# Kernel tuning notes

Hardware: AMD Instinct MI355X
Metric: run time of the kernel (lower is better)

## Reference

```python
import jax, jax.numpy as jnp
import numpy as np

N_EMBD = 1024
N_HEAD = 16
HEAD_DIM = N_EMBD // N_HEAD
B, T = 4, 1024
EPS = 1e-5


def _linear_params(key, fan_in, fan_out):
    kw, kb = jax.random.split(key)
    bound = 1.0 / np.sqrt(fan_in)
    W = jax.random.uniform(kw, (fan_in, fan_out), minval=-bound, maxval=bound, dtype=jnp.float32)
    b = jax.random.uniform(kb, (fan_out,), minval=-bound, maxval=bound, dtype=jnp.float32)
    return W, b


def setup_inputs() -> dict:
    key = jax.random.key(0)
    ks = jax.random.split(key, 8)
    x = jax.random.normal(ks[0], (B, T, N_EMBD), dtype=jnp.float32)
    Wq, bq = _linear_params(ks[1], N_EMBD, N_EMBD)
    Wk, bk = _linear_params(ks[2], N_EMBD, N_EMBD)
    Wv, bv = _linear_params(ks[3], N_EMBD, N_EMBD)
    Wp, bp = _linear_params(ks[4], N_EMBD, N_EMBD)
    W1, b1 = _linear_params(ks[5], N_EMBD, 4 * N_EMBD)
    W2, b2 = _linear_params(ks[6], 4 * N_EMBD, N_EMBD)
    g1 = jnp.ones((N_EMBD,), jnp.float32); be1 = jnp.zeros((N_EMBD,), jnp.float32)
    g2 = jnp.ones((N_EMBD,), jnp.float32); be2 = jnp.zeros((N_EMBD,), jnp.float32)
    return {"x": x, "Wq": Wq, "bq": bq, "Wk": Wk, "bk": bk, "Wv": Wv, "bv": bv,
            "Wp": Wp, "bp": bp, "W1": W1, "b1": b1, "W2": W2, "b2": b2,
            "g1": g1, "be1": be1, "g2": g2, "be2": be2}


def _layernorm(x, g, b):
    mu = jnp.mean(x, axis=-1, keepdims=True)
    var = jnp.mean(jnp.square(x - mu), axis=-1, keepdims=True)
    return (x - mu) * jax.lax.rsqrt(var + EPS) * g + b


def _attention(x, Wq, bq, Wk, bk, Wv, bv, Wp, bp):
    Bsz, Tt, C = x.shape
    def heads(W, b):
        return (x @ W + b).reshape(Bsz, Tt, N_HEAD, HEAD_DIM).transpose(0, 2, 1, 3)  # [B,H,T,d]
    q, k, v = heads(Wq, bq), heads(Wk, bk), heads(Wv, bv)
    scores = jnp.einsum('bhqd,bhkd->bhqk', q, k) / np.sqrt(HEAD_DIM).astype(np.float32)
    causal = jnp.tril(jnp.ones((Tt, Tt), dtype=bool))
    scores = jnp.where(causal, scores, -jnp.inf)
    attn = jax.nn.softmax(scores, axis=-1)
    out = jnp.einsum('bhqk,bhkd->bhqd', attn, v)  # [B,H,T,d]
    out = out.transpose(0, 2, 1, 3).reshape(Bsz, Tt, C)
    return out @ Wp + bp


def _ff(x, W1, b1, W2, b2):
    h = jax.nn.gelu(x @ W1 + b1, approximate=False)  # torch nn.GELU default = exact erf
    return h @ W2 + b2


def reference(x, Wq, bq, Wk, bk, Wv, bv, Wp, bp, W1, b1, W2, b2, g1, be1, g2, be2):
    x = x + _attention(_layernorm(x, g1, be1), Wq, bq, Wk, bk, Wv, bv, Wp, bp)
    x = x + _ff(_layernorm(x, g2, be2), W1, b1, W2, b2)
    return x
```

## Files before the change

kernel.cpp:

```cpp
#include <hip/hip_runtime.h>
#include <hip/hip_bf16.h>

typedef __attribute__((ext_vector_type(8))) __bf16 bf16x8;
typedef __attribute__((ext_vector_type(4))) float f32x4;
typedef __attribute__((ext_vector_type(4))) unsigned short u16x4;
typedef unsigned short u16;

#define AS3(p) ((__attribute__((address_space(3))) void*)(p))
#define AS1(p) ((const __attribute__((address_space(1))) void*)(p))

#define QSCALE 0.18033688011112042f

__device__ __forceinline__ u16 f2b(float f) {
    __hip_bfloat16 h = __float2bfloat16(f);
    return __builtin_bit_cast(u16, h);
}

__device__ __forceinline__ float gelu_exact(float v) {
    const float z = v * 0.70710678118654752f;
    const float a = fabsf(z);
    const float t = __builtin_amdgcn_rcpf(1.0f + 0.3275911f * a);
    float p = 1.061405429f;
    p = p * t - 1.453152027f;
    p = p * t + 1.421413741f;
    p = p * t - 0.284496736f;
    p = p * t + 0.254829592f;
    p = p * t;
    float erfv = 1.0f - p * __expf(-a * a);
    erfv = copysignf(erfv, z);
    return 0.5f * v * (1.0f + erfv);
}

__global__ __launch_bounds__(256) void transpose_w(
    const float* __restrict__ W, u16* __restrict__ WT, int K, int N)
{
    __shared__ u16 tile[32][33];
    const int tx = threadIdx.x & 31, ty = threadIdx.x >> 5;
    const int n0 = blockIdx.x * 32, k0 = blockIdx.y * 32;
    #pragma unroll
    for (int p = 0; p < 4; ++p)
        tile[ty + p * 8][tx] = f2b(W[(size_t)(k0 + ty + p * 8) * N + n0 + tx]);
    __syncthreads();
    #pragma unroll
    for (int p = 0; p < 4; ++p)
        WT[(size_t)(n0 + ty + p * 8) * K + k0 + tx] = tile[tx][ty + p * 8];
}

__global__ __launch_bounds__(256) void transpose_w3(
    const float* __restrict__ W0, const float* __restrict__ W1,
    const float* __restrict__ W2, u16* __restrict__ WT)
{
    __shared__ u16 tile[32][33];
    const int z = blockIdx.z;
    const float* W = (z == 0) ? W0 : (z == 1) ? W1 : W2;
    u16* dst = WT + (size_t)z * 1024 * 1024;
    const int tx = threadIdx.x & 31, ty = threadIdx.x >> 5;
    const int n0 = blockIdx.x * 32, k0 = blockIdx.y * 32;
    #pragma unroll
    for (int p = 0; p < 4; ++p)
        tile[ty + p * 8][tx] = f2b(W[(size_t)(k0 + ty + p * 8) * 1024 + n0 + tx]);
    __syncthreads();
    #pragma unroll
    for (int p = 0; p < 4; ++p)
        dst[(size_t)(n0 + ty + p * 8) * 1024 + k0 + tx] = tile[tx][ty + p * 8];
}

__global__ __launch_bounds__(256) void ln_bf16(
    const float* __restrict__ xin, const float* __restrict__ gam,
    const float* __restrict__ bet, u16* __restrict__ yout)
{
    __shared__ float red[8];
    const int row = blockIdx.x, tid = threadIdx.x;
    float4 v = ((const float4*)(xin + (size_t)row * 1024))[tid];
    float s = v.x + v.y + v.z + v.w;
    #pragma unroll
    for (int o = 32; o > 0; o >>= 1) s += __shfl_xor(s, o, 64);
    if ((tid & 63) == 0) red[tid >> 6] = s;
    __syncthreads();
    const float mu = (red[0] + red[1] + red[2] + red[3]) * (1.f / 1024.f);
    const float dx = v.x - mu, dy = v.y - mu, dz = v.z - mu, dw = v.w - mu;
    float sq = dx * dx + dy * dy + dz * dz + dw * dw;
    #pragma unroll
    for (int o = 32; o > 0; o >>= 1) sq += __shfl_xor(sq, o, 64);
    if ((tid & 63) == 0) red[4 + (tid >> 6)] = sq;
    __syncthreads();
    const float var = (red[4] + red[5] + red[6] + red[7]) * (1.f / 1024.f);
    const float inv = rsqrtf(var + 1e-5f);
    const float4 G = ((const float4*)gam)[tid];
    const float4 Bt = ((const float4*)bet)[tid];
    u16x4 o;
    o[0] = f2b(dx * inv * G.x + Bt.x);
    o[1] = f2b(dy * inv * G.y + Bt.y);
    o[2] = f2b(dz * inv * G.z + Bt.z);
    o[3] = f2b(dw * inv * G.w + Bt.w);
    ((u16x4*)(yout + (size_t)row * 1024))[tid] = o;
}

__global__ __launch_bounds__(256) void reduce_ln(
    const float* __restrict__ p0, const float* __restrict__ p1,
    const float* __restrict__ bias, const float* __restrict__ resid,
    const float* __restrict__ gam, const float* __restrict__ bet,
    float* __restrict__ xout, u16* __restrict__ yout)
{
    __shared__ float red[8];
    const int row = blockIdx.x, tid = threadIdx.x;
    const size_t off = (size_t)row * 256 + tid;
    float4 a = ((const float4*)p0)[off];
    const float4 b = ((const float4*)p1)[off];
    const float4 r = ((const float4*)resid)[off];
    const float4 bs = ((const float4*)bias)[tid];
    a.x += b.x + r.x + bs.x; a.y += b.y + r.y + bs.y;
    a.z += b.z + r.z + bs.z; a.w += b.w + r.w + bs.w;
    ((float4*)xout)[off] = a;
    float s = a.x + a.y + a.z + a.w;
    #pragma unroll
    for (int o = 32; o > 0; o >>= 1) s += __shfl_xor(s, o, 64);
    if ((tid & 63) == 0) red[tid >> 6] = s;
    __syncthreads();
    const float mu = (red[0] + red[1] + red[2] + red[3]) * (1.f / 1024.f);
    const float dx = a.x - mu, dy = a.y - mu, dz = a.z - mu, dw = a.w - mu;
    float sq = dx * dx + dy * dy + dz * dz + dw * dw;
    #pragma unroll
    for (int o = 32; o > 0; o >>= 1) sq += __shfl_xor(sq, o, 64);
    if ((tid & 63) == 0) red[4 + (tid >> 6)] = sq;
    __syncthreads();
    const float var = (red[4] + red[5] + red[6] + red[7]) * (1.f / 1024.f);
    const float inv = rsqrtf(var + 1e-5f);
    const float4 G = ((const float4*)gam)[tid];
    const float4 Bt = ((const float4*)bet)[tid];
    u16x4 o;
    o[0] = f2b(dx * inv * G.x + Bt.x);
    o[1] = f2b(dy * inv * G.y + Bt.y);
    o[2] = f2b(dz * inv * G.z + Bt.z);
    o[3] = f2b(dw * inv * G.w + Bt.w);
    ((u16x4*)(yout + (size_t)row * 1024))[tid] = o;
}

__global__ __launch_bounds__(256) void reduce_add(
    const float* __restrict__ p0, const float* __restrict__ p1,
    const float* __restrict__ bias, const float* __restrict__ resid,
    float* __restrict__ out)
{
    const size_t i = (size_t)blockIdx.x * 256 + threadIdx.x;
    float4 a = ((const float4*)p0)[i];
    const float4 b = ((const float4*)p1)[i];
    const float4 r = ((const float4*)resid)[i];
    const float4 bs = ((const float4*)bias)[i & 255];
    a.x += b.x + r.x + bs.x; a.y += b.y + r.y + bs.y;
    a.z += b.z + r.z + bs.z; a.w += b.w + r.w + bs.w;
    ((float4*)out)[i] = a;
}

template <int MODE, int BM, int SK>
__global__ __launch_bounds__(256, (BM == 128 ? 3 : 2)) void gemm_bf16(
    const u16* __restrict__ A, const u16* __restrict__ BT,
    const float* __restrict__ b0, const float* __restrict__ b1,
    const float* __restrict__ b2,
    void* __restrict__ outp, int M, int N, int K)
{
    constexpr int WM = BM / 2;
    constexpr int MI = WM / 16;
    constexpr int NI = 4;
    constexpr int AJ = BM / 64;
    constexpr int AELEM = BM * 32;
    constexpr int BELEM = 128 * 32;
    __shared__ u16 Asm[3 * AELEM];
    __shared__ u16 Bsm[3 * BELEM];

    const int tid = threadIdx.x;
    const int lane = tid & 63, wid = tid >> 6;
    const int wm = wid >> 1, wn = wid & 1;
    const int g = lane >> 4, l16 = lane & 15;
    const int sx = (l16 >> 1) & 3;
    const int sslot = (lane & 3) ^ ((lane >> 3) & 3);

    const int nBN = N >> 7;
    const int per = (M / BM) * nBN;
    const int cpx = gridDim.x >> 3;
    const int wg = (blockIdx.x & 7) * cpx + (blockIdx.x >> 3);
    const int skid = (SK > 1) ? (wg / per) : 0;
    const int rem = wg - skid * per;
    const int bm0 = (rem / nBN) * BM, bn0 = (rem % nBN) * 128;
    const int kb = skid * (K / SK);

    f32x4 acc[MI][NI] = {};

    const u16* aBase = A + (size_t)(bm0 + (lane >> 2)) * K + kb + sslot * 8;
    const u16* bBase = BT + (size_t)(bn0 + (lane >> 2)) * K + kb + sslot * 8;

    auto stage = [&](int kt, int buf) {
        u16* adst = Asm + buf * AELEM + lane * 8;
        u16* bdst = Bsm + buf * BELEM + lane * 8;
        #pragma unroll
        for (int j = 0; j < AJ; ++j) {
            const int ia = wid * AJ + j;
            __builtin_amdgcn_global_load_lds(AS1(aBase + (size_t)(ia * 16) * K + kt),
                                             AS3(adst + ia * 512), 16, 0, 0);
        }
        #pragma unroll
        for (int j = 0; j < 2; ++j) {
            const int ib = wid * 2 + j;
            __builtin_amdgcn_global_load_lds(AS1(bBase + (size_t)(ib * 16) * K + kt),
                                             AS3(bdst + ib * 512), 16, 0, 0);
        }
    };

    const int nt = K / (32 * SK);
    stage(0, 0);
    stage(32, 1);
    int cur = 0, pre = 2;

    for (int t = 0; t < nt; ++t) {
        if (t + 1 < nt) {
            if constexpr (BM == 256) asm volatile("s_waitcnt vmcnt(6)" ::: "memory");
            else                     asm volatile("s_waitcnt vmcnt(4)" ::: "memory");
        } else {
            asm volatile("s_waitcnt vmcnt(0)" ::: "memory");
        }
        __builtin_amdgcn_s_barrier();
        __builtin_amdgcn_sched_barrier(0);

        const u16* asrc = Asm + cur * AELEM;
        const u16* bsrc = Bsm + cur * BELEM;
        bf16x8 af[MI], bfr[NI];
        #pragma unroll
        for (int mi = 0; mi < MI; ++mi) {
            const int r = wm * WM + mi * 16 + l16;
            af[mi] = *(const bf16x8*)(asrc + r * 32 + ((g ^ sx) << 3));
        }
        #pragma unroll
        for (int ni = 0; ni < NI; ++ni) {
            const int c = wn * 64 + ni * 16 + l16;
            bfr[ni] = *(const bf16x8*)(bsrc + c * 32 + ((g ^ sx) << 3));
        }
        if (t + 2 < nt) stage((t + 2) * 32, pre);

        #pragma unroll
        for (int mi = 0; mi < MI; ++mi)
            #pragma unroll
            for (int ni = 0; ni < NI; ++ni)
                acc[mi][ni] = __builtin_amdgcn_mfma_f32_16x16x32_bf16(
                    af[mi], bfr[ni], acc[mi][ni], 0, 0, 0);

        pre = cur;
        cur = (cur == 2) ? 0 : cur + 1;
    }

    #pragma unroll
    for (int mi = 0; mi < MI; ++mi) {
        #pragma unroll
        for (int ni = 0; ni < NI; ++ni) {
            #pragma unroll
            for (int j = 0; j < 4; ++j) {
                const int m = bm0 + wm * WM + mi * 16 + g * 4 + j;
                const int n = bn0 + wn * 64 + ni * 16 + l16;
                float v = acc[mi][ni][j];
                if constexpr (MODE == 0) {
                    const float bias = (n < 1024) ? b0[n]
                                      : (n < 2048) ? b1[n - 1024] : b2[n - 2048];
                    float o = v + bias;
                    if (n < 1024) o *= QSCALE;
                    ((u16*)outp)[(size_t)m * N + n] = f2b(o);
                } else if constexpr (MODE == 2) {
                    ((u16*)outp)[(size_t)m * N + n] = f2b(gelu_exact(v + b0[n]));
                } else {
                    float* pout = (float*)outp + (size_t)skid * M * N;
                    pout[(size_t)m * N + n] = v;
                }
            }
        }
    }
}

__global__ __launch_bounds__(256) void attn_fwd(
    const u16* __restrict__ qkv, u16* __restrict__ outp)
{
    __shared__ u16 Ksm[2][64 * 64];
    __shared__ u16 Vsm[2][64 * 64];
    __shared__ u16 Psm[4][16 * 64];
    const int tid = threadIdx.x, lane = tid & 63, w = tid >> 6;
    const int lin = blockIdx.y * 8 + blockIdx.x;
    const int xq = (lin >> 3) & 7;
    const int bh = (((lin >> 6) & 7) << 3) | (lin & 7);
    const int b = bh >> 4, h = bh & 15;
    const int g = lane >> 4, l16 = lane & 15;
    const int skv = tid >> 4;
    const int sd4 = (tid & 15) * 4;

    const u16* kvb = qkv + (size_t)(b * 1024) * 3072 + 1024 + h * 64;

    bf16x8 vones;
    #pragma unroll
    for (int e = 0; e < 8; ++e) vones[e] = __builtin_bit_cast(__bf16, (u16)0x3F80);

    u16x4 kreg[4], vreg[4];
    auto issue = [&](int kv0) {
        const u16* kb = kvb + (size_t)kv0 * 3072;
        #pragma unroll
        for (int i = 0; i < 4; ++i)
            kreg[i] = *(const u16x4*)(kb + (size_t)(skv + 16 * i) * 3072 + sd4);
        #pragma unroll
        for (int i = 0; i < 4; ++i)
            vreg[i] = *(const u16x4*)(kb + (size_t)(4 * skv + i) * 3072 + 1024 + sd4);
    };
    auto stage_lds = [&](int buf) {
        #pragma unroll
        for (int i = 0; i < 4; ++i) {
            const int row = skv + 16 * i;
            *(u16x4*)(&Ksm[buf][row * 64 + (sd4 ^ ((row & 7) << 3))]) = kreg[i];
        }
        #pragma unroll
        for (int j = 0; j < 4; ++j) {
            u16x4 t;
            t[0] = vreg[0][j]; t[1] = vreg[1][j];
            t[2] = vreg[2][j]; t[3] = vreg[3][j];
            const int row = sd4 + j;
            *(u16x4*)(&Vsm[buf][row * 64 + ((4 * skv) ^ ((row & 7) << 3))]) = t;
        }
    };

    #pragma unroll
    for (int half = 0; half < 2; ++half) {
        const int qt = half ? (15 - xq) : xq;
        const int q0 = qt * 64;

        bf16x8 qf0, qf1;
        {
            const u16* qp = qkv + (size_t)(b * 1024 + q0 + w * 16 + l16) * 3072
                            + h * 64 + g * 8;
            qf0 = *(const bf16x8*)qp;
            qf1 = *(const bf16x8*)(qp + 32);
        }
        float m_run[4] = {-1e30f, -1e30f, -1e30f, -1e30f};
        float l_run[4] = {0.f, 0.f, 0.f, 0.f};
        f32x4 oacc[4] = {};

        issue(0);
        __syncthreads();
        stage_lds(0);
        if (qt > 0) issue(64);
        __syncthreads();
        int cur = 0;

        for (int kvt = 0; kvt <= qt; ++kvt) {
            f32x4 s[4];
            #pragma unroll
            for (int t = 0; t < 4; ++t) {
                const int r = t * 16 + l16;
                const int sw = (r & 7) << 3;
                const bf16x8 kf0 = *(const bf16x8*)(&Ksm[cur][r * 64 + ((g * 8) ^ sw)]);
                const bf16x8 kf1 = *(const bf16x8*)(&Ksm[cur][r * 64 + (((g + 4) * 8) ^ sw)]);
                f32x4 z = {};
                z = __builtin_amdgcn_mfma_f32_16x16x32_bf16(qf0, kf0, z, 0, 0, 0);
                z = __builtin_amdgcn_mfma_f32_16x16x32_bf16(qf1, kf1, z, 0, 0, 0);
                s[t] = z;
            }
            if (kvt == qt) {
                #pragma unroll
                for (int t = 0; t < 4; ++t)
                    #pragma unroll
                    for (int j = 0; j < 4; ++j) {
                        const int qrow = q0 + w * 16 + g * 4 + j;
                        const int kvc = q0 + t * 16 + l16;
                        if (kvc > qrow) s[t][j] = -1e30f;
                    }
            }
            float mx[4] = {-1e30f, -1e30f, -1e30f, -1e30f};
            #pragma unroll
            for (int t = 0; t < 4; ++t)
                #pragma unroll
                for (int j = 0; j < 4; ++j)
                    mx[j] = fmaxf(mx[j], s[t][j]);
            #pragma unroll
            for (int o = 1; o < 16; o <<= 1)
                #pragma unroll
                for (int j = 0; j < 4; ++j)
                    mx[j] = fmaxf(mx[j], __shfl_xor(mx[j], o, 16));
            float alpha[4];
            #pragma unroll
            for (int j = 0; j < 4; ++j) {
                const float mn = fmaxf(m_run[j], mx[j]);
                alpha[j] = __builtin_amdgcn_exp2f(m_run[j] - mn);
                m_run[j] = mn;
            }
            #pragma unroll
            for (int t = 0; t < 4; ++t)
                #pragma unroll
                for (int j = 0; j < 4; ++j)
                    s[t][j] = __builtin_amdgcn_exp2f(s[t][j] - m_run[j]);
            #pragma unroll
            for (int t = 0; t < 4; ++t)
                #pragma unroll
                for (int j = 0; j < 4; ++j) {
                    const int row = g * 4 + j;
                    Psm[w][row * 64 + ((t * 16 + l16) ^ ((row & 7) << 3))] = f2b(s[t][j]);
                }
            const int psw = (l16 & 7) << 3;
            const bf16x8 pf0 = *(const bf16x8*)(&Psm[w][l16 * 64 + ((g * 8) ^ psw)]);
            const bf16x8 pf1 = *(const bf16x8*)(&Psm[w][l16 * 64 + (((g + 4) * 8) ^ psw)]);
            f32x4 sum = {};
            sum = __builtin_amdgcn_mfma_f32_16x16x32_bf16(pf0, vones, sum, 0, 0, 0);
            sum = __builtin_amdgcn_mfma_f32_16x16x32_bf16(pf1, vones, sum, 0, 0, 0);
            #pragma unroll
            for (int j = 0; j < 4; ++j)
                l_run[j] = l_run[j] * alpha[j] + sum[j];
            #pragma unroll
            for (int dt = 0; dt < 4; ++dt)
                #pragma unroll
                for (int j = 0; j < 4; ++j)
                    oacc[dt][j] *= alpha[j];
            #pragma unroll
            for (int dt = 0; dt < 4; ++dt) {
                const int rv = dt * 16 + l16;
                const int sw = (rv & 7) << 3;
                const bf16x8 vf0 = *(const bf16x8*)(&Vsm[cur][rv * 64 + ((g * 8) ^ sw)]);
                const bf16x8 vf1 = *(const bf16x8*)(&Vsm[cur][rv * 64 + (((g + 4) * 8) ^ sw)]);
                oacc[dt] = __builtin_amdgcn_mfma_f32_16x16x32_bf16(pf0, vf0, oacc[dt], 0, 0, 0);
                oacc[dt] = __builtin_amdgcn_mfma_f32_16x16x32_bf16(pf1, vf1, oacc[dt], 0, 0, 0);
            }
            if (kvt < qt) {
                stage_lds(cur ^ 1);
                if (kvt + 2 <= qt) issue((kvt + 2) * 64);
                __syncthreads();
                cur ^= 1;
            }
        }
        #pragma unroll
        for (int j = 0; j < 4; ++j) l_run[j] = __builtin_amdgcn_rcpf(l_run[j]);
        #pragma unroll
        for (int dt = 0; dt < 4; ++dt)
            #pragma unroll
            for (int j = 0; j < 4; ++j) {
                const int m = b * 1024 + q0 + w * 16 + g * 4 + j;
                const int col = h * 64 + dt * 16 + l16;
                outp[(size_t)m * 1024 + col] = f2b(oacc[dt][j] * l_run[j]);
            }
    }
}

extern "C" void kernel_launch(void* const* d_in, const int* in_sizes, int n_in,
                              void* d_out, int out_size, void* d_ws, size_t ws_size,
                              hipStream_t stream)
{
    const float* x   = (const float*)d_in[0];
    const float* Wq  = (const float*)d_in[1];
    const float* bq  = (const float*)d_in[2];
    const float* Wk  = (const float*)d_in[3];
    const float* bk  = (const float*)d_in[4];
    const float* Wv  = (const float*)d_in[5];
    const float* bv  = (const float*)d_in[6];
    const float* Wp  = (const float*)d_in[7];
    const float* bp  = (const float*)d_in[8];
    const float* W1  = (const float*)d_in[9];
    const float* b1  = (const float*)d_in[10];
    const float* W2  = (const float*)d_in[11];
    const float* b2  = (const float*)d_in[12];
    const float* g1  = (const float*)d_in[13];
    const float* be1 = (const float*)d_in[14];
    const float* g2  = (const float*)d_in[15];
    const float* be2 = (const float*)d_in[16];

    char* ws = (char*)d_ws;
    const size_t MB = 1024 * 1024;
    u16*   ln_buf = (u16*)(ws);
    u16*   qkv    = (u16*)(ws + 8 * MB);
    u16*   attn_o = (u16*)(ws + 32 * MB);
    float* x1     = (float*)(ws + 40 * MB);
    u16*   hbuf   = (u16*)(ws + 56 * MB);
    u16*   wqkvT  = (u16*)(ws + 88 * MB);
    u16*   wpT    = (u16*)(ws + 94 * MB);
    u16*   w1T    = (u16*)(ws + 96 * MB);
    u16*   w2T    = (u16*)(ws + 104 * MB);
    float* projP  = (float*)(ws + 56 * MB);
    float* ff2P   = (float*)(ws + 8 * MB);

    transpose_w3<<<dim3(32, 32, 3), 256, 0, stream>>>(Wq, Wk, Wv, wqkvT);
    transpose_w<<<dim3(32, 32), 256, 0, stream>>>(Wp, wpT, 1024, 1024);
    transpose_w<<<dim3(128, 32), 256, 0, stream>>>(W1, w1T, 1024, 4096);
    transpose_w<<<dim3(32, 128), 256, 0, stream>>>(W2, w2T, 4096, 1024);

    ln_bf16<<<4096, 256, 0, stream>>>(x, g1, be1, ln_buf);
    gemm_bf16<0, 128, 1><<<768, 256, 0, stream>>>(
        ln_buf, wqkvT, bq, bk, bv, qkv, 4096, 3072, 1024);
    attn_fwd<<<dim3(8, 64), 256, 0, stream>>>(qkv, attn_o);
    gemm_bf16<3, 128, 2><<<512, 256, 0, stream>>>(
        attn_o, wpT, nullptr, nullptr, nullptr, projP, 4096, 1024, 1024);
    reduce_ln<<<4096, 256, 0, stream>>>(
        projP, projP + 4096 * 1024, bp, x, g2, be2, x1, ln_buf);
    gemm_bf16<2, 256, 1><<<512, 256, 0, stream>>>(
        ln_buf, w1T, b1, nullptr, nullptr, hbuf, 4096, 4096, 1024);
    gemm_bf16<3, 128, 2><<<512, 256, 0, stream>>>(
        hbuf, w2T, nullptr, nullptr, nullptr, ff2P, 4096, 1024, 4096);
    reduce_add<<<4096, 256, 0, stream>>>(
        ff2P, ff2P + 4096 * 1024, b2, x1, (float*)d_out);
}
```

Before: 212.3 us.

## Split GEMM K-step into two phases with staggered A/B prefetch and MFMA priority

The GEMM main loop now splits each K-tile into two halves. Each half loads part of the fragments, issues either the A or the B global-to-LDS prefetch, synchronises, and runs half of the MFMAs at raised wave priority via s_setprio. This is meant to interleave memory issue with matrix work and let waves in different phases overlap, in a ping-pong schedule. It adds extra barriers per iteration. The attention kernel also raises wave priority around its QK and PV MFMA blocks.

```diff
diff --git a/kernel.cpp b/kernel.cpp
--- a/kernel.cpp
+++ b/kernel.cpp
@@ -162,6 +162,7 @@
     constexpr int MI = WM / 16;
     constexpr int NI = 4;
     constexpr int AJ = BM / 64;
+    constexpr int LPS = AJ + 2;
     constexpr int AELEM = BM * 32;
     constexpr int BELEM = 128 * 32;
     __shared__ u16 Asm[3 * AELEM];
@@ -188,15 +189,17 @@
     const u16* aBase = A + (size_t)(bm0 + (lane >> 2)) * K + kb + sslot * 8;
     const u16* bBase = BT + (size_t)(bn0 + (lane >> 2)) * K + kb + sslot * 8;
 
-    auto stage = [&](int kt, int buf) {
+    auto stageA = [&](int kt, int buf) {
         u16* adst = Asm + buf * AELEM + lane * 8;
-        u16* bdst = Bsm + buf * BELEM + lane * 8;
         #pragma unroll
         for (int j = 0; j < AJ; ++j) {
             const int ia = wid * AJ + j;
             __builtin_amdgcn_global_load_lds(AS1(aBase + (size_t)(ia * 16) * K + kt),
                                              AS3(adst + ia * 512), 16, 0, 0);
         }
+    };
+    auto stageB = [&](int kt, int buf) {
+        u16* bdst = Bsm + buf * BELEM + lane * 8;
         #pragma unroll
         for (int j = 0; j < 2; ++j) {
             const int ib = wid * 2 + j;
@@ -206,42 +209,109 @@
     };
 
     const int nt = K / (32 * SK);
-    stage(0, 0);
-    stage(32, 1);
+    stageA(0, 0);  stageB(0, 0);
+    stageA(32, 1); stageB(32, 1);
+    if constexpr (LPS == 6) asm volatile("s_waitcnt vmcnt(6)" ::: "memory");
+    else                    asm volatile("s_waitcnt vmcnt(4)" ::: "memory");
+    __builtin_amdgcn_s_barrier();
+    __builtin_amdgcn_sched_barrier(0);
+
     int cur = 0, pre = 2;
 
     for (int t = 0; t < nt; ++t) {
-        if (t + 1 < nt) {
-            if constexpr (BM == 256) asm volatile("s_waitcnt vmcnt(6)" ::: "memory");
-            else                     asm volatile("s_waitcnt vmcnt(4)" ::: "memory");
-        } else {
-            asm volatile("s_waitcnt vmcnt(0)" ::: "memory");
-        }
-        __builtin_amdgcn_s_barrier();
-        __builtin_amdgcn_sched_barrier(0);
-
         const u16* asrc = Asm + cur * AELEM;
         const u16* bsrc = Bsm + cur * BELEM;
         bf16x8 af[MI], bfr[NI];
-        #pragma unroll
-        for (int mi = 0; mi < MI; ++mi) {
-            const int r = wm * WM + mi * 16 + l16;
-            af[mi] = *(const bf16x8*)(asrc + r * 32 + ((g ^ sx) << 3));
-        }
-        #pragma unroll
-        for (int ni = 0; ni < NI; ++ni) {
-            const int c = wn * 64 + ni * 16 + l16;
-            bfr[ni] = *(const bf16x8*)(bsrc + c * 32 + ((g ^ sx) << 3));
-        }
-        if (t + 2 < nt) stage((t + 2) * 32, pre);
-
-        #pragma unroll
-        for (int mi = 0; mi < MI; ++mi)
-            #pragma unroll
-            for (int ni = 0; ni < NI; ++ni)
-                acc[mi][ni] = __builtin_amdgcn_mfma_f32_16x16x32_bf16(
-                    af[mi], bfr[ni], acc[mi][ni], 0, 0, 0);
-
+
+        if constexpr (BM == 256) {
+            #pragma unroll
+            for (int mi = 0; mi < 4; ++mi) {
+                const int r = wm * WM + mi * 16 + l16;
+                af[mi] = *(const bf16x8*)(asrc + r * 32 + ((g ^ sx) << 3));
+            }
+            #pragma unroll
+            for (int ni = 0; ni < NI; ++ni) {
+                const int c = wn * 64 + ni * 16 + l16;
+                bfr[ni] = *(const bf16x8*)(bsrc + c * 32 + ((g ^ sx) << 3));
+            }
+        } else {
+            #pragma unroll
+            for (int mi = 0; mi < MI; ++mi) {
+                const int r = wm * WM + mi * 16 + l16;
+                af[mi] = *(const bf16x8*)(asrc + r * 32 + ((g ^ sx) << 3));
+            }
+            #pragma unroll
+            for (int ni = 0; ni < 2; ++ni) {
+                const int c = wn * 64 + ni * 16 + l16;
+                bfr[ni] = *(const bf16x8*)(bsrc + c * 32 + ((g ^ sx) << 3));
+            }
+        }
+        if (t + 2 < nt) stageA((t + 2) * 32, pre);
+        __builtin_amdgcn_s_barrier();
+        __builtin_amdgcn_sched_barrier(0);
+        __builtin_amdgcn_s_setprio(1);
+        if constexpr (BM == 256) {
+            #pragma unroll
+            for (int mi = 0; mi < 4; ++mi)
+                #pragma unroll
+                for (int ni = 0; ni < NI; ++ni)
+                    acc[mi][ni] = __builtin_amdgcn_mfma_f32_16x16x32_bf16(
+                        af[mi], bfr[ni], acc[mi][ni], 0, 0, 0);
+        } else {
+            #pragma unroll
+            for (int mi = 0; mi < MI; ++mi)
+                #pragma unroll
+                for (int ni = 0; ni < 2; ++ni)
+                    acc[mi][ni] = __builtin_amdgcn_mfma_f32_16x16x32_bf16(
+                        af[mi], bfr[ni], acc[mi][ni], 0, 0, 0);
+        }
+        __builtin_amdgcn_s_setprio(0);
+        __builtin_amdgcn_s_barrier();
+
+        if constexpr (BM == 256) {
+            #pragma unroll
+            for (int mi = 4; mi < 8; ++mi) {
+                const int r = wm * WM + mi * 16 + l16;
+                af[mi] = *(const bf16x8*)(asrc + r * 32 + ((g ^ sx) << 3));
+            }
+        } else {
+            #pragma unroll
+            for (int ni = 2; ni < 4; ++ni) {
+                const int c = wn * 64 + ni * 16 + l16;
+                bfr[ni] = *(const bf16x8*)(bsrc + c * 32 + ((g ^ sx) << 3));
+            }
+        }
+        if (t + 2 < nt) stageB((t + 2) * 32, pre);
+        __builtin_amdgcn_s_barrier();
+        __builtin_amdgcn_sched_barrier(0);
+        __builtin_amdgcn_s_setprio(1);
+        if constexpr (BM == 256) {
+            #pragma unroll
+            for (int mi = 4; mi < 8; ++mi)
+                #pragma unroll
+                for (int ni = 0; ni < NI; ++ni)
+                    acc[mi][ni] = __builtin_amdgcn_mfma_f32_16x16x32_bf16(
+                        af[mi], bfr[ni], acc[mi][ni], 0, 0, 0);
+        } else {
+            #pragma unroll
+            for (int mi = 0; mi < MI; ++mi)
+                #pragma unroll
+                for (int ni = 2; ni < 4; ++ni)
+                    acc[mi][ni] = __builtin_amdgcn_mfma_f32_16x16x32_bf16(
+                        af[mi], bfr[ni], acc[mi][ni], 0, 0, 0);
+        }
+        __builtin_amdgcn_s_setprio(0);
+
+        if (t + 1 < nt) {
+            if (t + 2 < nt) {
+                if constexpr (LPS == 6) asm volatile("s_waitcnt vmcnt(6)" ::: "memory");
+                else                    asm volatile("s_waitcnt vmcnt(4)" ::: "memory");
+            } else {
+                asm volatile("s_waitcnt vmcnt(0)" ::: "memory");
+            }
+            __builtin_amdgcn_s_barrier();
+            __builtin_amdgcn_sched_barrier(0);
+        }
         pre = cur;
         cur = (cur == 2) ? 0 : cur + 1;
     }
@@ -344,6 +414,7 @@
 
         for (int kvt = 0; kvt <= qt; ++kvt) {
             f32x4 s[4];
+            __builtin_amdgcn_s_setprio(1);
             #pragma unroll
             for (int t = 0; t < 4; ++t) {
                 const int r = t * 16 + l16;
@@ -355,6 +426,7 @@
                 z = __builtin_amdgcn_mfma_f32_16x16x32_bf16(qf1, kf1, z, 0, 0, 0);
                 s[t] = z;
             }
+            __builtin_amdgcn_s_setprio(0);
             if (kvt == qt) {
                 #pragma unroll
                 for (int t = 0; t < 4; ++t)
@@ -409,6 +481,7 @@
                 #pragma unroll
                 for (int j = 0; j < 4; ++j)
                     oacc[dt][j] *= alpha[j];
+            __builtin_amdgcn_s_setprio(1);
             #pragma unroll
             for (int dt = 0; dt < 4; ++dt) {
                 const int rv = dt * 16 + l16;
@@ -418,6 +491,7 @@
                 oacc[dt] = __builtin_amdgcn_mfma_f32_16x16x32_bf16(pf0, vf0, oacc[dt], 0, 0, 0);
                 oacc[dt] = __builtin_amdgcn_mfma_f32_16x16x32_bf16(pf1, vf1, oacc[dt], 0, 0, 0);
             }
+            __builtin_amdgcn_s_setprio(0);
             if (kvt < qt) {
                 stage_lds(cur ^ 1);
                 if (kvt + 2 <= qt) issue((kvt + 2) * 64);
```

Result: slower. 225.7 us (+6.3%).

## Use 3-way split-K for FF2, merge Wp transpose, prioritize attention MFMAs

Applied to the files above, without the earlier changes.

The FF2 GEMM moves from 2-way to 3-way split-K with 768 workgroups, aiming to fill the GPU's compute units in a single wave. Each split writes its own fp32 partial buffer, and a new reduce_add3 sums three partials plus bias and residual. Split-K ranges now handle a K that does not divide evenly. The Wp transpose joins the QKV transpose in one launch, and s_setprio raises wave priority around the attention MFMA blocks. The cost is an extra 16 MB partial buffer to write and read back, and that buffer reuses workspace that holds the transposed weights, which have already been consumed by the time it is written.

```diff
diff --git a/kernel.cpp b/kernel.cpp
--- a/kernel.cpp
+++ b/kernel.cpp
@@ -46,14 +46,15 @@
         WT[(size_t)(n0 + ty + p * 8) * K + k0 + tx] = tile[tx][ty + p * 8];
 }
 
-__global__ __launch_bounds__(256) void transpose_w3(
+__global__ __launch_bounds__(256) void transpose_w4(
     const float* __restrict__ W0, const float* __restrict__ W1,
-    const float* __restrict__ W2, u16* __restrict__ WT)
+    const float* __restrict__ W2, const float* __restrict__ W3,
+    u16* __restrict__ WTqkv, u16* __restrict__ WTp)
 {
     __shared__ u16 tile[32][33];
     const int z = blockIdx.z;
-    const float* W = (z == 0) ? W0 : (z == 1) ? W1 : W2;
-    u16* dst = WT + (size_t)z * 1024 * 1024;
+    const float* W = (z == 0) ? W0 : (z == 1) ? W1 : (z == 2) ? W2 : W3;
+    u16* dst = (z == 3) ? WTp : WTqkv + (size_t)z * 1024 * 1024;
     const int tx = threadIdx.x & 31, ty = threadIdx.x >> 5;
     const int n0 = blockIdx.x * 32, k0 = blockIdx.y * 32;
     #pragma unroll
@@ -136,18 +137,19 @@
     ((u16x4*)(yout + (size_t)row * 1024))[tid] = o;
 }
 
-__global__ __launch_bounds__(256) void reduce_add(
+__global__ __launch_bounds__(256) void reduce_add3(
     const float* __restrict__ p0, const float* __restrict__ p1,
-    const float* __restrict__ bias, const float* __restrict__ resid,
-    float* __restrict__ out)
+    const float* __restrict__ p2, const float* __restrict__ bias,
+    const float* __restrict__ resid, float* __restrict__ out)
 {
     const size_t i = (size_t)blockIdx.x * 256 + threadIdx.x;
     float4 a = ((const float4*)p0)[i];
     const float4 b = ((const float4*)p1)[i];
+    const float4 c = ((const float4*)p2)[i];
     const float4 r = ((const float4*)resid)[i];
     const float4 bs = ((const float4*)bias)[i & 255];
-    a.x += b.x + r.x + bs.x; a.y += b.y + r.y + bs.y;
-    a.z += b.z + r.z + bs.z; a.w += b.w + r.w + bs.w;
+    a.x += b.x + c.x + r.x + bs.x; a.y += b.y + c.y + r.y + bs.y;
+    a.z += b.z + c.z + r.z + bs.z; a.w += b.w + c.w + r.w + bs.w;
     ((float4*)out)[i] = a;
 }
 
@@ -181,12 +183,16 @@
     const int skid = (SK > 1) ? (wg / per) : 0;
     const int rem = wg - skid * per;
     const int bm0 = (rem / nBN) * BM, bn0 = (rem % nBN) * 128;
-    const int kb = skid * (K / SK);
+
+    const int tsteps = K >> 5;
+    const int sbase = tsteps / SK, srem = tsteps % SK;
+    const int nt = sbase + (skid < srem ? 1 : 0);
+    const int kstart = (skid * sbase + (skid < srem ? skid : srem)) << 5;
 
     f32x4 acc[MI][NI] = {};
 
-    const u16* aBase = A + (size_t)(bm0 + (lane >> 2)) * K + kb + sslot * 8;
-    const u16* bBase = BT + (size_t)(bn0 + (lane >> 2)) * K + kb + sslot * 8;
+    const u16* aBase = A + (size_t)(bm0 + (lane >> 2)) * K + kstart + sslot * 8;
+    const u16* bBase = BT + (size_t)(bn0 + (lane >> 2)) * K + kstart + sslot * 8;
 
     auto stage = [&](int kt, int buf) {
         u16* adst = Asm + buf * AELEM + lane * 8;
@@ -205,7 +211,6 @@
         }
     };
 
-    const int nt = K / (32 * SK);
     stage(0, 0);
     stage(32, 1);
     int cur = 0, pre = 2;
@@ -264,7 +269,7 @@
                 } else if constexpr (MODE == 2) {
                     ((u16*)outp)[(size_t)m * N + n] = f2b(gelu_exact(v + b0[n]));
                 } else {
-                    float* pout = (float*)outp + (size_t)skid * M * N;
+                    float* pout = (float*)(skid == 0 ? b0 : skid == 1 ? b1 : b2);
                     pout[(size_t)m * N + n] = v;
                 }
             }
@@ -344,6 +349,7 @@
 
         for (int kvt = 0; kvt <= qt; ++kvt) {
             f32x4 s[4];
+            __builtin_amdgcn_s_setprio(1);
             #pragma unroll
             for (int t = 0; t < 4; ++t) {
                 const int r = t * 16 + l16;
@@ -355,6 +361,7 @@
                 z = __builtin_amdgcn_mfma_f32_16x16x32_bf16(qf1, kf1, z, 0, 0, 0);
                 s[t] = z;
             }
+            __builtin_amdgcn_s_setprio(0);
             if (kvt == qt) {
                 #pragma unroll
                 for (int t = 0; t < 4; ++t)
@@ -409,6 +416,7 @@
                 #pragma unroll
                 for (int j = 0; j < 4; ++j)
                     oacc[dt][j] *= alpha[j];
+            __builtin_amdgcn_s_setprio(1);
             #pragma unroll
             for (int dt = 0; dt < 4; ++dt) {
                 const int rv = dt * 16 + l16;
@@ -418,6 +426,7 @@
                 oacc[dt] = __builtin_amdgcn_mfma_f32_16x16x32_bf16(pf0, vf0, oacc[dt], 0, 0, 0);
                 oacc[dt] = __builtin_amdgcn_mfma_f32_16x16x32_bf16(pf1, vf1, oacc[dt], 0, 0, 0);
             }
+            __builtin_amdgcn_s_setprio(0);
             if (kvt < qt) {
                 stage_lds(cur ^ 1);
                 if (kvt + 2 <= qt) issue((kvt + 2) * 64);
@@ -471,11 +480,13 @@
     u16*   wpT    = (u16*)(ws + 94 * MB);
     u16*   w1T    = (u16*)(ws + 96 * MB);
     u16*   w2T    = (u16*)(ws + 104 * MB);
-    float* projP  = (float*)(ws + 56 * MB);
-    float* ff2P   = (float*)(ws + 8 * MB);
-
-    transpose_w3<<<dim3(32, 32, 3), 256, 0, stream>>>(Wq, Wk, Wv, wqkvT);
-    transpose_w<<<dim3(32, 32), 256, 0, stream>>>(Wp, wpT, 1024, 1024);
+    float* projP0 = (float*)(ws + 56 * MB);
+    float* projP1 = (float*)(ws + 72 * MB);
+    float* ff2P0  = (float*)(ws + 8 * MB);
+    float* ff2P1  = (float*)(ws + 24 * MB);
+    float* ff2P2  = (float*)(ws + 88 * MB);
+
+    transpose_w4<<<dim3(32, 32, 4), 256, 0, stream>>>(Wq, Wk, Wv, Wp, wqkvT, wpT);
     transpose_w<<<dim3(128, 32), 256, 0, stream>>>(W1, w1T, 1024, 4096);
     transpose_w<<<dim3(32, 128), 256, 0, stream>>>(W2, w2T, 4096, 1024);
 
@@ -484,13 +495,13 @@
         ln_buf, wqkvT, bq, bk, bv, qkv, 4096, 3072, 1024);
     attn_fwd<<<dim3(8, 64), 256, 0, stream>>>(qkv, attn_o);
     gemm_bf16<3, 128, 2><<<512, 256, 0, stream>>>(
-        attn_o, wpT, nullptr, nullptr, nullptr, projP, 4096, 1024, 1024);
+        attn_o, wpT, projP0, projP1, nullptr, nullptr, 4096, 1024, 1024);
     reduce_ln<<<4096, 256, 0, stream>>>(
-        projP, projP + 4096 * 1024, bp, x, g2, be2, x1, ln_buf);
+        projP0, projP1, bp, x, g2, be2, x1, ln_buf);
     gemm_bf16<2, 256, 1><<<512, 256, 0, stream>>>(
         ln_buf, w1T, b1, nullptr, nullptr, hbuf, 4096, 4096, 1024);
-    gemm_bf16<3, 128, 2><<<512, 256, 0, stream>>>(
-        hbuf, w2T, nullptr, nullptr, nullptr, ff2P, 4096, 1024, 4096);
-    reduce_add<<<4096, 256, 0, stream>>>(
-        ff2P, ff2P + 4096 * 1024, b2, x1, (float*)d_out);
-}
+    gemm_bf16<3, 128, 3><<<768, 256, 0, stream>>>(
+        hbuf, w2T, ff2P0, ff2P1, ff2P2, nullptr, 4096, 1024, 4096);
+    reduce_add3<<<4096, 256, 0, stream>>>(
+        ff2P0, ff2P1, ff2P2, b2, x1, (float*)d_out);
+}
```

Result: no change. 215.9 us (+1.7%).
